# Kernel optimization log

Measured on AMD Instinct MI355X. Metric: run time of the kernel, lower is better.

## Reference

```python
import jax, jax.numpy as jnp
import numpy as np

N_NODES = 100000
N_EDGES = 600000
N_RBF = 6
EMBED_DIM = 128
VOCAB = 100  # nn.Embedding(100, embed_dim, padding_idx=0)


def setup_inputs() -> dict:
    key = jax.random.key(0)
    k1, k2, k3, k4, k5, k6, k7 = jax.random.split(key, 7)
    e_rbf = jax.random.normal(k1, (N_EDGES, N_RBF), dtype=jnp.float32)
    z = jax.random.randint(k2, (N_NODES,), 0, VOCAB, dtype=jnp.int64)
    nbr_list = jax.random.randint(k3, (N_EDGES, 2), 0, N_NODES, dtype=jnp.int64)
    # params
    W_edge = jax.random.normal(k4, (N_RBF, EMBED_DIM), dtype=jnp.float32) / np.sqrt(N_RBF)
    emb_table = jax.random.normal(k5, (VOCAB, EMBED_DIM), dtype=jnp.float32)
    emb_table = emb_table.at[0].set(0.0)  # padding_idx=0
    W_dense = jax.random.normal(k6, (3 * EMBED_DIM, EMBED_DIM), dtype=jnp.float32) / np.sqrt(3 * EMBED_DIM)
    b_dense = jax.random.normal(k7, (EMBED_DIM,), dtype=jnp.float32) * 0.01
    return {"e_rbf": e_rbf, "z": z, "nbr_list": nbr_list,
            "W_edge": W_edge, "emb_table": emb_table,
            "W_dense": W_dense, "b_dense": b_dense}


def reference(e_rbf, z, nbr_list, W_edge, emb_table, W_dense, b_dense):
    # edge_dense: [E, n_rbf] @ [n_rbf, D] -> [E, D], no bias, no activation
    e = e_rbf @ W_edge
    # node embedding lookup: [N, D]
    h = emb_table[z]
    # gather + concat: [E, 3D]
    m_ji = jnp.concatenate((h[nbr_list[:, 0]], h[nbr_list[:, 1]], e), axis=-1)
    # dense 3D -> D with bias, then swish (silu) activation
    m_ji = jax.nn.silu(m_ji @ W_dense + b_dense)
    return m_ji
```

## Files before the change

kernel.cpp:

```cpp
#include <hip/hip_runtime.h>

#define EMBED 128
#define NRBF 6
#define VOCAB 100
#define EBLOCK 1024
#define GROUPS 32
#define CPG 37
#define HALF (GROUPS * CPG)
#define BCHUNK (2 * HALF)
#define TABLE_F (VOCAB * EMBED * 2 + NRBF * EMBED)
#define RBF_F (HALF * NRBF)
#define SMEM_BYTES ((TABLE_F + RBF_F) * 4 + HALF * 4)

__global__ __launch_bounds__(EMBED) void precompute_kernel(
    const float* __restrict__ W_edge,
    const float* __restrict__ emb,
    const float* __restrict__ Wd,
    const float* __restrict__ b,
    float* __restrict__ T1,
    float* __restrict__ T2,
    float* __restrict__ Wc)
{
    const int d = threadIdx.x;
    const int v = blockIdx.x;
    if (v < VOCAB) {
        __shared__ float hrow[EMBED];
        hrow[d] = emb[v * EMBED + d];
        __syncthreads();
        float acc1 = b[d];
        float acc2 = 0.0f;
        #pragma unroll 8
        for (int j = 0; j < EMBED; ++j) {
            const float hv = hrow[j];
            acc1 += hv * Wd[j * EMBED + d];
            acc2 += hv * Wd[(EMBED + j) * EMBED + d];
        }
        T1[v * EMBED + d] = acc1;
        T2[v * EMBED + d] = acc2;
    } else {
        const int k = v - VOCAB;
        float acc = 0.0f;
        #pragma unroll 8
        for (int j = 0; j < EMBED; ++j)
            acc += W_edge[k * EMBED + j] * Wd[(2 * EMBED + j) * EMBED + d];
        Wc[k * EMBED + d] = acc;
    }
}

__global__ __launch_bounds__(EBLOCK) void edge_kernel(
    const float* __restrict__ e_rbf,
    const int*   __restrict__ z,
    const int*   __restrict__ nbr,
    const float* __restrict__ tables,
    float* __restrict__ out,
    int E)
{
    extern __shared__ float smem[];
    float* T1s    = smem;
    float* T2s    = smem + VOCAB * EMBED;
    float* Wcs    = smem + 2 * VOCAB * EMBED;
    float* rbf_s  = smem + TABLE_F;
    int*   desc_s = (int*)(smem + TABLE_F + RBF_F);

    const int tid  = threadIdx.x;
    const int base = blockIdx.x * BCHUNK;
    const int lane = tid & 31;
    const int d    = lane * 4;
    const int g    = tid >> 5;

    const float4* erbf4 = reinterpret_cast<const float4*>(e_rbf);
    const int nf4 = (int)(((long)E * NRBF) >> 2);

    {
        const float4* src = reinterpret_cast<const float4*>(tables);
        float4* dst = reinterpret_cast<float4*>(smem);
        #pragma unroll 2
        for (int i = tid; i < TABLE_F / 4; i += EBLOCK)
            dst[i] = src[i];
    }
    {
        const int src0 = (base * NRBF) >> 2;
        float4* dst = reinterpret_cast<float4*>(rbf_s);
        #pragma unroll 2
        for (int i = tid; i < RBF_F / 4; i += EBLOCK) {
            const int s = src0 + i;
            dst[i] = (s < nf4) ? erbf4[s] : make_float4(0.f, 0.f, 0.f, 0.f);
        }
        #pragma unroll 2
        for (int i = tid; i < HALF; i += EBLOCK) {
            const int e = base + i;
            if (e < E) {
                const int2 nn = *reinterpret_cast<const int2*>(nbr + 2 * e);
                desc_s[i] = z[nn.x] | (z[nn.y] << 16);
            }
        }
    }
    __syncthreads();

    const float4 wc0 = *reinterpret_cast<const float4*>(Wcs + 0 * EMBED + d);
    const float4 wc1 = *reinterpret_cast<const float4*>(Wcs + 1 * EMBED + d);
    const float4 wc2 = *reinterpret_cast<const float4*>(Wcs + 2 * EMBED + d);
    const float4 wc3 = *reinterpret_cast<const float4*>(Wcs + 3 * EMBED + d);
    const float4 wc4 = *reinterpret_cast<const float4*>(Wcs + 4 * EMBED + d);
    const float4 wc5 = *reinterpret_cast<const float4*>(Wcs + 5 * EMBED + d);

    auto compute_half = [&](int ebase) {
        const int lbase = g * CPG;
        #pragma unroll 4
        for (int i = 0; i < CPG; ++i) {
            const int e = ebase + lbase + i;
            if (e >= E) break;
            const unsigned dsc = (unsigned)desc_s[lbase + i];
            const int za = (int)(dsc & 0xffffu) << 7;
            const int zb = (int)(dsc >> 16) << 7;

            const float* rp = rbf_s + (lbase + i) * NRBF;
            const float2 f01 = *reinterpret_cast<const float2*>(rp + 0);
            const float2 f23 = *reinterpret_cast<const float2*>(rp + 2);
            const float2 f45 = *reinterpret_cast<const float2*>(rp + 4);

            float4 acc = *reinterpret_cast<const float4*>(T1s + za + d);
            const float4 t2 = *reinterpret_cast<const float4*>(T2s + zb + d);
            acc.x += t2.x; acc.y += t2.y; acc.z += t2.z; acc.w += t2.w;

            acc.x += f01.x * wc0.x; acc.y += f01.x * wc0.y; acc.z += f01.x * wc0.z; acc.w += f01.x * wc0.w;
            acc.x += f01.y * wc1.x; acc.y += f01.y * wc1.y; acc.z += f01.y * wc1.z; acc.w += f01.y * wc1.w;
            acc.x += f23.x * wc2.x; acc.y += f23.x * wc2.y; acc.z += f23.x * wc2.z; acc.w += f23.x * wc2.w;
            acc.x += f23.y * wc3.x; acc.y += f23.y * wc3.y; acc.z += f23.y * wc3.z; acc.w += f23.y * wc3.w;
            acc.x += f45.x * wc4.x; acc.y += f45.x * wc4.y; acc.z += f45.x * wc4.z; acc.w += f45.x * wc4.w;
            acc.x += f45.y * wc5.x; acc.y += f45.y * wc5.y; acc.z += f45.y * wc5.z; acc.w += f45.y * wc5.w;

            float4 rr;
            rr.x = acc.x * __builtin_amdgcn_rcpf(1.0f + __expf(-acc.x));
            rr.y = acc.y * __builtin_amdgcn_rcpf(1.0f + __expf(-acc.y));
            rr.z = acc.z * __builtin_amdgcn_rcpf(1.0f + __expf(-acc.z));
            rr.w = acc.w * __builtin_amdgcn_rcpf(1.0f + __expf(-acc.w));

            *reinterpret_cast<float4*>(out + (long)e * EMBED + d) = rr;
        }
    };

    compute_half(base);
    __syncthreads();

    {
        const int src0 = ((base + HALF) * NRBF) >> 2;
        float4* dst = reinterpret_cast<float4*>(rbf_s);
        #pragma unroll 2
        for (int i = tid; i < RBF_F / 4; i += EBLOCK) {
            const int s = src0 + i;
            dst[i] = (s < nf4) ? erbf4[s] : make_float4(0.f, 0.f, 0.f, 0.f);
        }
        #pragma unroll 2
        for (int i = tid; i < HALF; i += EBLOCK) {
            const int e = base + HALF + i;
            if (e < E) {
                const int2 nn = *reinterpret_cast<const int2*>(nbr + 2 * e);
                desc_s[i] = z[nn.x] | (z[nn.y] << 16);
            }
        }
    }
    __syncthreads();

    compute_half(base + HALF);
}

extern "C" void kernel_launch(void* const* d_in, const int* in_sizes, int n_in,
                              void* d_out, int out_size, void* d_ws, size_t ws_size,
                              hipStream_t stream)
{
    const float* e_rbf  = (const float*)d_in[0];
    const int*   z      = (const int*)  d_in[1];
    const int*   nbr    = (const int*)  d_in[2];
    const float* W_edge = (const float*)d_in[3];
    const float* emb    = (const float*)d_in[4];
    const float* Wd     = (const float*)d_in[5];
    const float* b      = (const float*)d_in[6];
    float* out = (float*)d_out;

    const int E = in_sizes[2] / 2;

    float* T1 = (float*)d_ws;
    float* T2 = T1 + VOCAB * EMBED;
    float* Wc = T2 + VOCAB * EMBED;

    precompute_kernel<<<VOCAB + NRBF, EMBED, 0, stream>>>(W_edge, emb, Wd, b, T1, T2, Wc);

    const int grid = (E + BCHUNK - 1) / BCHUNK;
    edge_kernel<<<grid, EBLOCK, SMEM_BYTES, stream>>>(e_rbf, z, nbr, T1, out, E);
}
```

Before: 83.04 us.

## Prefetch second-half edge metadata into registers and pack rbf as fp16

The edge kernel now packs each edge's six rbf values (as fp16) and its two atom types into one 16-byte shared record. It issues the global loads for the second half-chunk into registers before the first half is computed, so that load latency overlaps with compute. The per-group edge assignment is interleaved, and the precompute kernel is split across twice as many blocks for more parallelism. Rounding the rbf inputs to fp16 reduces accuracy of the edge term, and the extra live registers may lower occupancy.

```diff
diff --git a/kernel.cpp b/kernel.cpp
--- a/kernel.cpp
+++ b/kernel.cpp
@@ -1,4 +1,5 @@
 #include <hip/hip_runtime.h>
+#include <hip/hip_fp16.h>
 
 #define EMBED 128
 #define NRBF 6
@@ -9,8 +10,7 @@
 #define HALF (GROUPS * CPG)
 #define BCHUNK (2 * HALF)
 #define TABLE_F (VOCAB * EMBED * 2 + NRBF * EMBED)
-#define RBF_F (HALF * NRBF)
-#define SMEM_BYTES ((TABLE_F + RBF_F) * 4 + HALF * 4)
+#define SMEM_BYTES (TABLE_F * 4 + HALF * 16)
 
 __global__ __launch_bounds__(EMBED) void precompute_kernel(
     const float* __restrict__ W_edge,
@@ -23,22 +23,20 @@
 {
     const int d = threadIdx.x;
     const int v = blockIdx.x;
-    if (v < VOCAB) {
+    if (v < 2 * VOCAB) {
+        const int row = (v < VOCAB) ? v : v - VOCAB;
+        const int woff = (v < VOCAB) ? 0 : EMBED;
         __shared__ float hrow[EMBED];
-        hrow[d] = emb[v * EMBED + d];
+        hrow[d] = emb[row * EMBED + d];
         __syncthreads();
-        float acc1 = b[d];
-        float acc2 = 0.0f;
+        float acc = (v < VOCAB) ? b[d] : 0.0f;
         #pragma unroll 8
-        for (int j = 0; j < EMBED; ++j) {
-            const float hv = hrow[j];
-            acc1 += hv * Wd[j * EMBED + d];
-            acc2 += hv * Wd[(EMBED + j) * EMBED + d];
-        }
-        T1[v * EMBED + d] = acc1;
-        T2[v * EMBED + d] = acc2;
+        for (int j = 0; j < EMBED; ++j)
+            acc += hrow[j] * Wd[(woff + j) * EMBED + d];
+        if (v < VOCAB) T1[row * EMBED + d] = acc;
+        else           T2[row * EMBED + d] = acc;
     } else {
-        const int k = v - VOCAB;
+        const int k = v - 2 * VOCAB;
         float acc = 0.0f;
         #pragma unroll 8
         for (int j = 0; j < EMBED; ++j)
@@ -56,20 +54,16 @@
     int E)
 {
     extern __shared__ float smem[];
-    float* T1s    = smem;
-    float* T2s    = smem + VOCAB * EMBED;
-    float* Wcs    = smem + 2 * VOCAB * EMBED;
-    float* rbf_s  = smem + TABLE_F;
-    int*   desc_s = (int*)(smem + TABLE_F + RBF_F);
+    float* T1s = smem;
+    float* T2s = smem + VOCAB * EMBED;
+    float* Wcs = smem + 2 * VOCAB * EMBED;
+    uint4* meta = (uint4*)(smem + TABLE_F);
 
     const int tid  = threadIdx.x;
     const int base = blockIdx.x * BCHUNK;
     const int lane = tid & 31;
     const int d    = lane * 4;
     const int g    = tid >> 5;
-
-    const float4* erbf4 = reinterpret_cast<const float4*>(e_rbf);
-    const int nf4 = (int)(((long)E * NRBF) >> 2);
 
     {
         const float4* src = reinterpret_cast<const float4*>(tables);
@@ -78,22 +72,52 @@
         for (int i = tid; i < TABLE_F / 4; i += EBLOCK)
             dst[i] = src[i];
     }
+
     {
-        const int src0 = (base * NRBF) >> 2;
-        float4* dst = reinterpret_cast<float4*>(rbf_s);
-        #pragma unroll 2
-        for (int i = tid; i < RBF_F / 4; i += EBLOCK) {
-            const int s = src0 + i;
-            dst[i] = (s < nf4) ? erbf4[s] : make_float4(0.f, 0.f, 0.f, 0.f);
-        }
-        #pragma unroll 2
-        for (int i = tid; i < HALF; i += EBLOCK) {
-            const int e = base + i;
+        for (int s = 0; s < 2; ++s) {
+            const int idx = tid + s * EBLOCK;
+            if (idx >= HALF) break;
+            const int e = base + idx;
+            uint4 m = make_uint4(0u, 0u, 0u, 0u);
             if (e < E) {
                 const int2 nn = *reinterpret_cast<const int2*>(nbr + 2 * e);
-                desc_s[i] = z[nn.x] | (z[nn.y] << 16);
+                const float* rp = e_rbf + (long)e * NRBF;
+                const float2 a = *reinterpret_cast<const float2*>(rp + 0);
+                const float2 bb = *reinterpret_cast<const float2*>(rp + 2);
+                const float2 c = *reinterpret_cast<const float2*>(rp + 4);
+                __half2 ha = __float22half2_rn(a);
+                __half2 hb = __float22half2_rn(bb);
+                __half2 hc = __float22half2_rn(c);
+                m.x = *reinterpret_cast<unsigned*>(&ha);
+                m.y = *reinterpret_cast<unsigned*>(&hb);
+                m.z = *reinterpret_cast<unsigned*>(&hc);
+                m.w = (unsigned)z[nn.x] | ((unsigned)z[nn.y] << 16);
             }
-        }
+            meta[idx] = m;
+        }
+    }
+
+    int2  nnA = make_int2(0, 0);
+    float2 rA0 = make_float2(0.f, 0.f), rA1 = rA0, rA2 = rA0;
+    int2  nnB = make_int2(0, 0);
+    float2 rB0 = make_float2(0.f, 0.f), rB1 = rB0, rB2 = rB0;
+    const int eA = base + HALF + tid;
+    const bool vA = (eA < E);
+    const int eB = base + HALF + EBLOCK + tid;
+    const bool vB = (tid < HALF - EBLOCK) && (eB < E);
+    if (vA) {
+        nnA = *reinterpret_cast<const int2*>(nbr + 2 * eA);
+        const float* rp = e_rbf + (long)eA * NRBF;
+        rA0 = *reinterpret_cast<const float2*>(rp + 0);
+        rA1 = *reinterpret_cast<const float2*>(rp + 2);
+        rA2 = *reinterpret_cast<const float2*>(rp + 4);
+    }
+    if (vB) {
+        nnB = *reinterpret_cast<const int2*>(nbr + 2 * eB);
+        const float* rp = e_rbf + (long)eB * NRBF;
+        rB0 = *reinterpret_cast<const float2*>(rp + 0);
+        rB1 = *reinterpret_cast<const float2*>(rp + 2);
+        rB2 = *reinterpret_cast<const float2*>(rp + 4);
     }
     __syncthreads();
 
@@ -104,20 +128,20 @@
     const float4 wc4 = *reinterpret_cast<const float4*>(Wcs + 4 * EMBED + d);
     const float4 wc5 = *reinterpret_cast<const float4*>(Wcs + 5 * EMBED + d);
 
-    auto compute_half = [&](int ebase) {
-        const int lbase = g * CPG;
+    auto consume_half = [&](int ebase) {
+        const int lb = (g >> 1) * (2 * CPG) + (g & 1);
         #pragma unroll 4
         for (int i = 0; i < CPG; ++i) {
-            const int e = ebase + lbase + i;
+            const int le = lb + 2 * i;
+            const int e = ebase + le;
             if (e >= E) break;
-            const unsigned dsc = (unsigned)desc_s[lbase + i];
-            const int za = (int)(dsc & 0xffffu) << 7;
-            const int zb = (int)(dsc >> 16) << 7;
-
-            const float* rp = rbf_s + (lbase + i) * NRBF;
-            const float2 f01 = *reinterpret_cast<const float2*>(rp + 0);
-            const float2 f23 = *reinterpret_cast<const float2*>(rp + 2);
-            const float2 f45 = *reinterpret_cast<const float2*>(rp + 4);
+
+            const uint4 m = meta[le];
+            const float2 f01 = __half22float2(*reinterpret_cast<const __half2*>(&m.x));
+            const float2 f23 = __half22float2(*reinterpret_cast<const __half2*>(&m.y));
+            const float2 f45 = __half22float2(*reinterpret_cast<const __half2*>(&m.z));
+            const int za = (int)(m.w & 0xffffu) << 7;
+            const int zb = (int)(m.w >> 16) << 7;
 
             float4 acc = *reinterpret_cast<const float4*>(T1s + za + d);
             const float4 t2 = *reinterpret_cast<const float4*>(T2s + zb + d);
@@ -140,29 +164,40 @@
         }
     };
 
-    compute_half(base);
+    consume_half(base);
     __syncthreads();
 
     {
-        const int src0 = ((base + HALF) * NRBF) >> 2;
-        float4* dst = reinterpret_cast<float4*>(rbf_s);
-        #pragma unroll 2
-        for (int i = tid; i < RBF_F / 4; i += EBLOCK) {
-            const int s = src0 + i;
-            dst[i] = (s < nf4) ? erbf4[s] : make_float4(0.f, 0.f, 0.f, 0.f);
-        }
-        #pragma unroll 2
-        for (int i = tid; i < HALF; i += EBLOCK) {
-            const int e = base + HALF + i;
-            if (e < E) {
-                const int2 nn = *reinterpret_cast<const int2*>(nbr + 2 * e);
-                desc_s[i] = z[nn.x] | (z[nn.y] << 16);
+        if (tid < HALF) {
+            uint4 m = make_uint4(0u, 0u, 0u, 0u);
+            if (vA) {
+                __half2 ha = __float22half2_rn(rA0);
+                __half2 hb = __float22half2_rn(rA1);
+                __half2 hc = __float22half2_rn(rA2);
+                m.x = *reinterpret_cast<unsigned*>(&ha);
+                m.y = *reinterpret_cast<unsigned*>(&hb);
+                m.z = *reinterpret_cast<unsigned*>(&hc);
+                m.w = (unsigned)z[nnA.x] | ((unsigned)z[nnA.y] << 16);
             }
+            meta[tid] = m;
+        }
+        if (tid < HALF - EBLOCK) {
+            uint4 m = make_uint4(0u, 0u, 0u, 0u);
+            if (vB) {
+                __half2 ha = __float22half2_rn(rB0);
+                __half2 hb = __float22half2_rn(rB1);
+                __half2 hc = __float22half2_rn(rB2);
+                m.x = *reinterpret_cast<unsigned*>(&ha);
+                m.y = *reinterpret_cast<unsigned*>(&hb);
+                m.z = *reinterpret_cast<unsigned*>(&hc);
+                m.w = (unsigned)z[nnB.x] | ((unsigned)z[nnB.y] << 16);
+            }
+            meta[EBLOCK + tid] = m;
         }
     }
     __syncthreads();
 
-    compute_half(base + HALF);
+    consume_half(base + HALF);
 }
 
 extern "C" void kernel_launch(void* const* d_in, const int* in_sizes, int n_in,
@@ -184,7 +219,7 @@
     float* T2 = T1 + VOCAB * EMBED;
     float* Wc = T2 + VOCAB * EMBED;
 
-    precompute_kernel<<<VOCAB + NRBF, EMBED, 0, stream>>>(W_edge, emb, Wd, b, T1, T2, Wc);
+    precompute_kernel<<<2 * VOCAB + NRBF, EMBED, 0, stream>>>(W_edge, emb, Wd, b, T1, T2, Wc);
 
     const int grid = (E + BCHUNK - 1) / BCHUNK;
     edge_kernel<<<grid, EBLOCK, SMEM_BYTES, stream>>>(e_rbf, z, nbr, T1, out, E);
```

Result: faster. 78.96 us (-4.9%).
